# Kernel optimization log

Measured on AMD Instinct MI355X. Metric: run time of the kernel, lower is better.

Reference implementation:

```python
import jax, jax.numpy as jnp
import numpy as np

CONF_THRES = 0.8
NMS_THRES = 0.4
MAX_DET = 300          # fixed capacity for jit-compatible NMS output
N_BOXES = 262144
N_CLASSES = 80


def xywh2xyxy(x):
    xy, wh = x[..., :2], x[..., 2:4]
    return jnp.concatenate([xy - wh * 0.5, xy + wh * 0.5], axis=-1)


def bbox_iou(box, boxes):
    # one box [4] vs many [N,4]; original uses the +1 pixel-area convention
    x1 = jnp.maximum(box[0], boxes[:, 0])
    y1 = jnp.maximum(box[1], boxes[:, 1])
    x2 = jnp.minimum(box[2], boxes[:, 2])
    y2 = jnp.minimum(box[3], boxes[:, 3])
    inter = jnp.clip(x2 - x1 + 1, 0) * jnp.clip(y2 - y1 + 1, 0)
    a1 = (box[2] - box[0] + 1) * (box[3] - box[1] + 1)
    a2 = (boxes[:, 2] - boxes[:, 0] + 1) * (boxes[:, 3] - boxes[:, 1] + 1)
    return inter / (a1 + a2 - inter + 1e-16)


def nms_single(pred):
    # pred: [N, 85] raw YOLO output for one image
    boxes = xywh2xyxy(pred[:, :4])
    obj = pred[:, 4]
    cls_scores = pred[:, 5:]
    class_conf = cls_scores.max(axis=-1)
    class_pred = jnp.argmax(cls_scores, axis=-1).astype(pred.dtype)
    valid = obj >= CONF_THRES
    score = obj * class_conf
    # sort valid boxes by descending score; invalid pushed to the end
    order = jnp.argsort(jnp.where(valid, -score, jnp.inf))
    det = jnp.concatenate(
        [boxes, obj[:, None], class_conf[:, None], class_pred[:, None]], axis=1
    )[order]  # [N, 7] = x1,y1,x2,y2,obj,class_conf,class_pred
    valid = valid[order]

    def step(valid, _):
        idx = jnp.argmax(valid)            # first still-valid (= highest score)
        any_valid = jnp.any(valid)
        cur = det[idx]
        iou = bbox_iou(cur[:4], det[:, :4])
        invalid = (iou > NMS_THRES) & (det[:, 6] == cur[6]) & valid
        # weighted box merge over the suppressed group (as in original NMS)
        w = jnp.where(invalid, det[:, 4], 0.0)
        merged = (w[:, None] * det[:, :4]).sum(0) / (w.sum() + 1e-16)
        out = jnp.where(any_valid,
                        jnp.concatenate([merged, cur[4:]]),
                        jnp.zeros(7, pred.dtype))
        return valid & ~invalid, (out, any_valid)

    _, (kept, kept_valid) = jax.lax.scan(step, valid, None, length=MAX_DET)
    return kept, kept_valid  # [MAX_DET,7], [MAX_DET]


def setup_inputs() -> dict:
    key = jax.random.key(0)
    detections = jax.random.uniform(key, (1, N_BOXES, 5 + N_CLASSES), dtype=jnp.float32)
    return {"detections": detections}


def reference(detections):
    kept, kv = nms_single(detections[0])
    d = kept[:, 5:]                        # [MAX_DET, 2] = (class_conf, class_pred)
    conf_key = jnp.where(kv, d[:, 0], -jnp.inf)  # padded rows sort to the end
    order = jnp.argsort(conf_key)          # ascending (torch argsort)
    d = d[order][::-1]                     # torch.flip -> descending class_conf
    kv = kv[order][::-1]
    probs = jnp.where(kv, d[:, 0], 0.0)    # self.probs
    ids = d[:, 1][None, :]                 # self.ids, shape [1, MAX_DET]
    return ids, probs
```

## Files before the change

kernel.cpp:

```cpp
#include <hip/hip_runtime.h>

#pragma clang fp contract(off)

#define NBOX 262144
#define NCLS 80
#define ROWS 85
#define CAP 1024
#define NSUB 8
#define SUBCAP 128
#define POOL 8192
#define BPT 2
#define S1BOX 512

typedef unsigned long long ull;

__global__ __launch_bounds__(1024) void k_init(int* __restrict__ cnt_pad,
                                               int* __restrict__ pool_count,
                                               int* __restrict__ done_count) {
    const int t = threadIdx.x;
    for (int i = t; i < NCLS * NSUB * 16; i += 1024) cnt_pad[i] = 0;
    if (t == 0) { *pool_count = 0; *done_count = 0; }
}

__global__ __launch_bounds__(256) void k_stage1(const float* __restrict__ det,
                                                int* __restrict__ cnt_pad,
                                                ull* __restrict__ key2,
                                                float* __restrict__ conf2,
                                                float4* __restrict__ box2) {
    __shared__ int s_wl[S1BOX];
    __shared__ float s_obj[S1BOX];
    __shared__ int s_nv;
    const int t = threadIdx.x;
    const int b0 = blockIdx.x * S1BOX;
    const int sb = blockIdx.x & (NSUB - 1);

    if (t == 0) s_nv = 0;
    __syncthreads();

    float obj[BPT];
    #pragma unroll
    for (int i = 0; i < BPT; i++)
        obj[i] = det[(size_t)(b0 + (i << 8) + t) * ROWS + 4];
    #pragma unroll
    for (int i = 0; i < BPT; i++) {
        if (obj[i] >= 0.8f) {
            int r = atomicAdd(&s_nv, 1);
            s_wl[r] = (i << 8) + t;
            s_obj[r] = obj[i];
        }
    }
    __syncthreads();
    const int nv = s_nv;

    const int grp = t >> 4, c = t & 15;
    const int lane = t & 63;
    #pragma unroll 2
    for (int r0 = 0; r0 < nv; r0 += 16) {
        int widx = r0 + grp;
        if (widx < nv) {
            int b = s_wl[widx];
            const float* p = det + (size_t)(b0 + b) * ROWS;
            float aux = (c < 5) ? p[c] : 0.0f;
            float v0 = p[5 + c];
            float v1 = p[21 + c];
            float v2 = p[37 + c];
            float v3 = p[53 + c];
            float v4 = p[69 + c];
            float mv = v0; int mj = c;
            if (v1 > mv) { mv = v1; mj = 16 + c; }
            if (v2 > mv) { mv = v2; mj = 32 + c; }
            if (v3 > mv) { mv = v3; mj = 48 + c; }
            if (v4 > mv) { mv = v4; mj = 64 + c; }
            #pragma unroll
            for (int off = 8; off; off >>= 1) {
                float ov = __shfl_xor(mv, off);
                int oj = __shfl_xor(mj, off);
                if (ov > mv || (ov == mv && oj < mj)) { mv = ov; mj = oj; }
            }
            int gb = lane & 48;
            float x = __shfl(aux, gb + 0);
            float y = __shfl(aux, gb + 1);
            float w = __shfl(aux, gb + 2);
            float h = __shfl(aux, gb + 3);
            if (c == 0) {
                float ob = s_obj[widx];
                float score = ob * mv;
                float hw = w * 0.5f, hh = h * 0.5f;
                int gi = b0 + b;
                int r = atomicAdd(&cnt_pad[((mj * NSUB + sb) << 4)], 1);
                if (r < SUBCAP) {
                    int pos = (mj << 10) + (sb << 7) + r;
                    key2[pos] = ((ull)(~__float_as_uint(score)) << 32) | (unsigned)gi;
                    conf2[pos] = mv;
                    box2[pos] = make_float4(x - hw, y - hh, x + hw, y + hh);
                }
            }
        }
    }
}

template <int L>
__device__ __forceinline__ int exact_alive(ull (&k)[L]) {
    int a = 0;
    #pragma unroll
    for (int j = 0; j < L; j++) a += (int)__popcll(__ballot(k[j] != ~0ULL));
    return a;
}

template <int L>
__device__ __forceinline__ void pick_loop(ull (&k)[L], float4 (&bx)[L], float (&cf)[L],
                                          float (&ar)[L],
                                          int lane, int& alive, int& np,
                                          ull* pkey, float* pconf, int stopAt) {
    while (alive > stopAt && np < 300) {
        ull lm = k[0]; int lj = 0;
        #pragma unroll
        for (int j = 1; j < L; j++) if (k[j] < lm) { lm = k[j]; lj = j; }
        ull gm = lm;
        #pragma unroll
        for (int off = 32; off; off >>= 1) { ull o = __shfl_xor(gm, off); if (o < gm) gm = o; }
        if (gm == ~0ULL) { alive = 0; break; }
        float4 cb = bx[0]; float cc = cf[0];
        #pragma unroll
        for (int j = 1; j < L; j++) if (j == lj) { cb = bx[j]; cc = cf[j]; }
        ull wb = __ballot(lm == gm);
        int wl2 = (int)__ffsll((long long)wb) - 1;
        cb.x = __shfl(cb.x, wl2); cb.y = __shfl(cb.y, wl2);
        cb.z = __shfl(cb.z, wl2); cb.w = __shfl(cb.w, wl2);
        cc = __shfl(cc, wl2);
        if (lane == 0) { pkey[np] = gm; pconf[np] = cc; }
        np++;
        float a1 = (cb.z - cb.x + 1.0f) * (cb.w - cb.y + 1.0f);
        #pragma unroll
        for (int j = 0; j < L; j++) {
            if (k[j] != ~0ULL) {
                float4 b = bx[j];
                float xx1 = fmaxf(cb.x, b.x), yy1 = fmaxf(cb.y, b.y);
                float xx2 = fminf(cb.z, b.z), yy2 = fminf(cb.w, b.w);
                float iw = xx2 - xx1 + 1.0f, ih = yy2 - yy1 + 1.0f;
                float inter = fmaxf(iw, 0.0f) * fmaxf(ih, 0.0f);
                float iou = inter / (a1 + ar[j] - inter + 1e-16f);
                if (iou > 0.4f) k[j] = ~0ULL;
            }
        }
        if ((np & 7) == 0) alive = exact_alive(k);
    }
}

template <int LF, int LT>
__device__ __forceinline__ void compact_regs(ull (&k)[LF], float4 (&bx)[LF], float (&cf)[LF],
                                             ull (&k2)[LT], float4 (&b2)[LT], float (&c2)[LT],
                                             float (&a2)[LT],
                                             int lane, int alive,
                                             ull* dk, float4* db, float* dc) {
    int ci = 0;
    #pragma unroll
    for (int j = 0; j < LF; j++) if (k[j] != ~0ULL) ci++;
    int inc = ci;
    for (int off = 1; off < 64; off <<= 1) {
        int o = __shfl_up(inc, off);
        if (lane >= off) inc += o;
    }
    int wp = inc - ci;
    #pragma unroll
    for (int j = 0; j < LF; j++)
        if (k[j] != ~0ULL) { dk[wp] = k[j]; db[wp] = bx[j]; dc[wp] = cf[j]; wp++; }
    #pragma unroll
    for (int j = 0; j < LT; j++) {
        int pos = lane + (j << 6);
        bool ok = pos < alive;
        k2[j] = ok ? dk[pos] : ~0ULL;
        b2[j] = ok ? db[pos] : make_float4(0.f, 0.f, 0.f, 0.f);
        c2[j] = ok ? dc[pos] : 0.0f;
        a2[j] = (b2[j].z - b2[j].x + 1.0f) * (b2[j].w - b2[j].y + 1.0f);
    }
}

__device__ __forceinline__ void bsort512(ull (&x)[8], int lane) {
    #pragma unroll
    for (int k = 2; k <= 512; k <<= 1) {
        #pragma unroll
        for (int j = k >> 1; j >= 64; j >>= 1) {
            const int jr = j >> 6;
            #pragma unroll
            for (int r2 = 0; r2 < 8; r2++) {
                if ((r2 & jr) == 0) {
                    const bool asc = (((r2 << 6) & k) == 0);
                    ull a = x[r2], b = x[r2 | jr];
                    if ((a > b) == asc) { x[r2] = b; x[r2 | jr] = a; }
                }
            }
        }
        #pragma unroll
        for (int j = ((k >> 1) > 32 ? 32 : (k >> 1)); j >= 1; j >>= 1) {
            #pragma unroll
            for (int r2 = 0; r2 < 8; r2++) {
                int i = (r2 << 6) + lane;
                bool asc = ((i & k) == 0);
                ull o = __shfl_xor(x[r2], j);
                bool lower = ((lane & j) == 0);
                ull mn = x[r2] < o ? x[r2] : o;
                ull mx2 = x[r2] < o ? o : x[r2];
                x[r2] = (asc == lower) ? mn : mx2;
            }
        }
    }
}

__global__ __launch_bounds__(256) void k_nmsfinal(const int* __restrict__ cnt_pad,
                                                  const ull* __restrict__ key2,
                                                  const float* __restrict__ conf2,
                                                  const float4* __restrict__ box2,
                                                  ull* __restrict__ pool_key,
                                                  float* __restrict__ pool_conf,
                                                  int* __restrict__ pool_cls,
                                                  int* __restrict__ pool_count,
                                                  int* __restrict__ done_count,
                                                  float* __restrict__ out) {
    __shared__ ull sk[CAP];
    __shared__ float4 sbx[CAP];
    __shared__ float scf[CAP];
    __shared__ ull pkey[CAP];
    __shared__ float pconf[CAP];
    __shared__ int s_fin;
    __shared__ int s_hist[256];
    __shared__ int s_wt[4];
    __shared__ int s_stat[4];
    __shared__ ull s_buf[512];
    __shared__ unsigned s_cb[512];
    __shared__ unsigned s_cl[512];

    const int c = blockIdx.x, t = threadIdx.x, lane = t & 63, wave = t >> 6;

    if (wave == 0) {
        const int s0 = c << 10;
        int cv0 = 0;
        if (lane < NSUB) cv0 = min(cnt_pad[((c * NSUB + lane) << 4)], SUBCAP);
        int ntot = cv0;
        #pragma unroll
        for (int off = 32; off; off >>= 1) ntot += __shfl_xor(ntot, off);

        ull k16[16]; float4 b16[16]; float c16[16]; float a16[16];
        #pragma unroll
        for (int j = 0; j < 16; j++) {
            int pos = lane + (j << 6);
            int sub = pos >> 7;
            int lim = __shfl(cv0, sub);
            bool ok = (pos & (SUBCAP - 1)) < lim;
            k16[j] = ok ? key2[s0 + pos] : ~0ULL;
            b16[j] = ok ? box2[s0 + pos] : make_float4(0.f, 0.f, 0.f, 0.f);
            c16[j] = ok ? conf2[s0 + pos] : 0.0f;
            a16[j] = (b16[j].z - b16[j].x + 1.0f) * (b16[j].w - b16[j].y + 1.0f);
        }
        int alive = ntot, np = 0;
        pick_loop<16>(k16, b16, c16, a16, lane, alive, np, pkey, pconf, 256);
        alive = exact_alive(k16);
        ull k4[4]; float4 b4[4]; float c4[4]; float a4[4];
        compact_regs<16, 4>(k16, b16, c16, k4, b4, c4, a4, lane, alive, sk, sbx, scf);
        pick_loop<4>(k4, b4, c4, a4, lane, alive, np, pkey, pconf, 64);
        alive = exact_alive(k4);
        ull k1[1]; float4 b1[1]; float c1[1]; float a1r[1];
        compact_regs<4, 1>(k4, b4, c4, k1, b1, c1, a1r, lane, alive, sk, sbx, scf);
        pick_loop<1>(k1, b1, c1, a1r, lane, alive, np, pkey, pconf, 0);

        int npw = min(np, 300);
        int base = 0;
        if (lane == 0 && npw) base = atomicAdd(pool_count, npw);
        base = __shfl(base, 0);
        for (int j = lane; j < npw; j += 64) {
            int pp = base + j;
            if (pp < POOL) {
                ull gm = pkey[j];
                ull pk = ((ull)((unsigned)(gm >> 32) & 0x7FFFFFFFu) << 32)
                       | ((gm & 0xFFFFFFFFull) << 14) | (ull)pp;
                __hip_atomic_store(&pool_key[pp], pk,
                                   __ATOMIC_RELAXED, __HIP_MEMORY_SCOPE_AGENT);
                __hip_atomic_store(&pool_conf[pp], pconf[j],
                                   __ATOMIC_RELAXED, __HIP_MEMORY_SCOPE_AGENT);
                __hip_atomic_store(&pool_cls[pp], c,
                                   __ATOMIC_RELAXED, __HIP_MEMORY_SCOPE_AGENT);
            }
        }
        asm volatile("s_waitcnt vmcnt(0)" ::: "memory");
    }
    __syncthreads();
    if (t == 0) {
        int ticket = atomicAdd(done_count, 1);
        s_fin = (ticket == NCLS - 1) ? 1 : 0;
    }
    __syncthreads();
    if (!s_fin) return;

    const int K = min(__hip_atomic_load(pool_count, __ATOMIC_RELAXED,
                                        __HIP_MEMORY_SCOPE_AGENT), POOL);
    ull key[32];
    #pragma unroll
    for (int j = 0; j < 32; j++) {
        int pos = t + (j << 8);
        key[j] = (pos < K) ? __hip_atomic_load(&pool_key[pos], __ATOMIC_RELAXED,
                                               __HIP_MEMORY_SCOPE_AGENT)
                           : ~0ULL;
    }

    const bool selAll = (K <= 511);
    int sh = 55;
    ull pfin = 0;
    if (!selAll) {
        ull p = 0;
        int gBelow = 0, r = 300;
        while (true) {
            s_hist[t] = 0;
            __syncthreads();
            #pragma unroll
            for (int j = 0; j < 32; j++) {
                ull kk = key[j];
                if ((kk >> (sh + 8)) == p)
                    atomicAdd(&s_hist[(int)((kk >> sh) & 0xFFull)], 1);
            }
            __syncthreads();
            int v = s_hist[t];
            int incv = v;
            for (int off = 1; off < 64; off <<= 1) {
                int o = __shfl_up(incv, off);
                if (lane >= off) incv += o;
            }
            if (lane == 63) s_wt[wave] = incv;
            __syncthreads();
            int wo = 0;
            #pragma unroll
            for (int w2 = 0; w2 < 4; w2++) if (w2 < wave) wo += s_wt[w2];
            int cumIncl = wo + incv;
            int cumExcl = cumIncl - v;
            if (cumExcl < r && r <= cumIncl) {
                s_stat[0] = t; s_stat[1] = cumExcl; s_stat[2] = cumIncl;
            }
            __syncthreads();
            int D = s_stat[0], below = s_stat[1], incl = s_stat[2];
            if (gBelow + incl <= 511 || sh == 7) {
                pfin = (p << 8) | (ull)D;
                break;
            }
            p = (p << 8) | (ull)D;
            gBelow += below;
            r = 300 - gBelow;
            sh -= 8;
            __syncthreads();
        }
    }

    if (t == 0) s_stat[3] = 0;
    __syncthreads();
    int ci = 0;
    #pragma unroll
    for (int j = 0; j < 32; j++) {
        ull kk = key[j];
        bool sel = selAll ? ((kk >> 63) == 0) : ((kk >> sh) <= pfin);
        if (sel) ci++;
    }
    int inc = ci;
    for (int off = 1; off < 64; off <<= 1) {
        int o = __shfl_up(inc, off);
        if (lane >= off) inc += o;
    }
    int wtot = __shfl(inc, 63);
    int wbase2 = 0;
    if (lane == 0 && wtot) wbase2 = atomicAdd(&s_stat[3], wtot);
    wbase2 = __shfl(wbase2, 0);
    int wp = wbase2 + inc - ci;
    #pragma unroll
    for (int j = 0; j < 32; j++) {
        ull kk = key[j];
        bool sel = selAll ? ((kk >> 63) == 0) : ((kk >> sh) <= pfin);
        if (sel) s_buf[wp++] = kk;
    }
    __syncthreads();
    const int S = s_stat[3];
    for (int i = t; i < 512; i += 256) if (i >= S) s_buf[i] = ~0ULL;
    __syncthreads();
    if (wave != 0) return;

    #pragma clang loop unroll(disable)
    for (int pass = 0; pass < 2; pass++) {
        ull x[8];
        #pragma unroll
        for (int r2 = 0; r2 < 8; r2++) x[r2] = s_buf[(r2 << 6) + lane];
        bsort512(x, lane);
        if (pass == 0) {
            #pragma unroll
            for (int r2 = 0; r2 < 8; r2++) {
                int i = (r2 << 6) + lane;
                ull kk = x[r2];
                ull k2 = ~0ULL;
                if (i < 300 && kk != ~0ULL) {
                    int pidx = (int)(kk & 0x3FFFull);
                    unsigned cb = __float_as_uint(
                        __hip_atomic_load(&pool_conf[pidx], __ATOMIC_RELAXED,
                                          __HIP_MEMORY_SCOPE_AGENT));
                    unsigned cl = (unsigned)__hip_atomic_load(&pool_cls[pidx],
                                          __ATOMIC_RELAXED, __HIP_MEMORY_SCOPE_AGENT);
                    s_cb[i] = cb; s_cl[i] = cl;
                    k2 = ((ull)(~cb) << 32) | (unsigned)(~i);
                }
                s_buf[i] = k2;
            }
        } else {
            #pragma unroll
            for (int r2 = 0; r2 < 8; r2++) {
                int i = (r2 << 6) + lane;
                if (i < 300) {
                    ull kk = x[r2];
                    float idv = 0.0f, pv = 0.0f;
                    if (kk != ~0ULL) {
                        int slot = (int)(~(unsigned)(kk & 0xFFFFFFFFull));
                        pv = __uint_as_float(s_cb[slot]);
                        idv = (float)(int)s_cl[slot];
                    }
                    out[i] = idv;
                    out[300 + i] = pv;
                }
            }
        }
    }
}

extern "C" void kernel_launch(void* const* d_in, const int* in_sizes, int n_in,
                              void* d_out, int out_size, void* d_ws, size_t ws_size,
                              hipStream_t stream) {
    const float* det = (const float*)d_in[0];
    float* out = (float*)d_out;
    char* ws = (char*)d_ws;

    int* cnt_pad = (int*)(ws + 0);
    int* pool_count = (int*)(ws + 40960);
    int* done_count = (int*)(ws + 40964);
    ull* key2 = (ull*)(ws + 41024);
    float* conf2 = (float*)(ws + 696384);
    float4* box2 = (float4*)(ws + 1024064);
    ull* pool_key = (ull*)(ws + 2334784);
    float* pool_conf = (float*)(ws + 2400320);
    int* pool_cls = (int*)(ws + 2433088);

    k_init<<<1, 1024, 0, stream>>>(cnt_pad, pool_count, done_count);
    k_stage1<<<NBOX / S1BOX, 256, 0, stream>>>(det, cnt_pad, key2, conf2, box2);
    k_nmsfinal<<<NCLS, 256, 0, stream>>>(cnt_pad, key2, conf2, box2,
                                         pool_key, pool_conf, pool_cls, pool_count,
                                         done_count, out);
}
```

Baseline: 181.7 us.

## Speed up per-class NMS pick loop with tree argmin and 32-bit wave reduce

The per-lane argmin in the NMS pick loop becomes a tree reduction, and the cross-lane min reduces on the high 32 bits of the key first. It falls back to a full 64-bit reduction only when several lanes tie or nothing is left. Input loads are now issued unconditionally before the count read so memory latency overlaps, and the final 4-to-1 compaction stage is dropped in favour of running the 4-wide loop to completion. Shared arrays are also shrunk. The aim is a shorter serial dependency chain per pick, at the cost of more branching and loads of unused slots.

```diff
diff --git a/kernel.cpp b/kernel.cpp
--- a/kernel.cpp
+++ b/kernel.cpp
@@ -113,18 +113,44 @@
                                           int lane, int& alive, int& np,
                                           ull* pkey, float* pconf, int stopAt) {
     while (alive > stopAt && np < 300) {
-        ull lm = k[0]; int lj = 0;
-        #pragma unroll
-        for (int j = 1; j < L; j++) if (k[j] < lm) { lm = k[j]; lj = j; }
-        ull gm = lm;
-        #pragma unroll
-        for (int off = 32; off; off >>= 1) { ull o = __shfl_xor(gm, off); if (o < gm) gm = o; }
-        if (gm == ~0ULL) { alive = 0; break; }
+        ull v[L]; int ix[L];
+        #pragma unroll
+        for (int j = 0; j < L; j++) { v[j] = k[j]; ix[j] = j; }
+        #pragma unroll
+        for (int s = L >> 1; s; s >>= 1) {
+            #pragma unroll
+            for (int j = 0; j < s; j++)
+                if (v[j + s] < v[j]) { v[j] = v[j + s]; ix[j] = ix[j + s]; }
+        }
+        ull lm = v[0]; const int lj = ix[0];
         float4 cb = bx[0]; float cc = cf[0];
         #pragma unroll
         for (int j = 1; j < L; j++) if (j == lj) { cb = bx[j]; cc = cf[j]; }
-        ull wb = __ballot(lm == gm);
-        int wl2 = (int)__ffsll((long long)wb) - 1;
+        unsigned lo = (unsigned)lm;
+        unsigned hi = (unsigned)(lm >> 32);
+        unsigned mh = hi;
+        #pragma unroll
+        for (int off = 32; off; off >>= 1) {
+            unsigned o = __shfl_xor(mh, off);
+            mh = o < mh ? o : mh;
+        }
+        ull wb = __ballot(hi == mh);
+        ull gm; int wl2;
+        if (mh == 0xFFFFFFFFu || __popcll(wb) != 1) {
+            ull g = (hi == mh) ? lm : ~0ULL;
+            #pragma unroll
+            for (int off = 32; off; off >>= 1) {
+                ull o = __shfl_xor(g, off);
+                if (o < g) g = o;
+            }
+            gm = g;
+            if (gm == ~0ULL) { alive = 0; break; }
+            wb = __ballot(lm == gm);
+            wl2 = (int)__ffsll((long long)wb) - 1;
+        } else {
+            wl2 = (int)__ffsll((long long)wb) - 1;
+            gm = ((ull)mh << 32) | (ull)__shfl(lo, wl2);
+        }
         cb.x = __shfl(cb.x, wl2); cb.y = __shfl(cb.y, wl2);
         cb.z = __shfl(cb.z, wl2); cb.w = __shfl(cb.w, wl2);
         cc = __shfl(cc, wl2);
@@ -147,15 +173,14 @@
     }
 }
 
-template <int LF, int LT>
-__device__ __forceinline__ void compact_regs(ull (&k)[LF], float4 (&bx)[LF], float (&cf)[LF],
-                                             ull (&k2)[LT], float4 (&b2)[LT], float (&c2)[LT],
-                                             float (&a2)[LT],
+__device__ __forceinline__ void compact16to4(ull (&k)[16], float4 (&bx)[16], float (&cf)[16],
+                                             ull (&k2)[4], float4 (&b2)[4], float (&c2)[4],
+                                             float (&a2)[4],
                                              int lane, int alive,
                                              ull* dk, float4* db, float* dc) {
     int ci = 0;
     #pragma unroll
-    for (int j = 0; j < LF; j++) if (k[j] != ~0ULL) ci++;
+    for (int j = 0; j < 16; j++) if (k[j] != ~0ULL) ci++;
     int inc = ci;
     for (int off = 1; off < 64; off <<= 1) {
         int o = __shfl_up(inc, off);
@@ -163,10 +188,10 @@
     }
     int wp = inc - ci;
     #pragma unroll
-    for (int j = 0; j < LF; j++)
+    for (int j = 0; j < 16; j++)
         if (k[j] != ~0ULL) { dk[wp] = k[j]; db[wp] = bx[j]; dc[wp] = cf[j]; wp++; }
     #pragma unroll
-    for (int j = 0; j < LT; j++) {
+    for (int j = 0; j < 4; j++) {
         int pos = lane + (j << 6);
         bool ok = pos < alive;
         k2[j] = ok ? dk[pos] : ~0ULL;
@@ -217,11 +242,11 @@
                                                   int* __restrict__ pool_count,
                                                   int* __restrict__ done_count,
                                                   float* __restrict__ out) {
-    __shared__ ull sk[CAP];
-    __shared__ float4 sbx[CAP];
-    __shared__ float scf[CAP];
-    __shared__ ull pkey[CAP];
-    __shared__ float pconf[CAP];
+    __shared__ ull sk[256];
+    __shared__ float4 sbx[256];
+    __shared__ float scf[256];
+    __shared__ ull pkey[304];
+    __shared__ float pconf[304];
     __shared__ int s_fin;
     __shared__ int s_hist[256];
     __shared__ int s_wt[4];
@@ -234,34 +259,41 @@
 
     if (wave == 0) {
         const int s0 = c << 10;
+        ull k16[16]; float4 b16[16]; float c16[16]; float a16[16];
+        #pragma unroll
+        for (int j = 0; j < 16; j++) {
+            int pos = lane + (j << 6);
+            k16[j] = key2[s0 + pos];
+            b16[j] = box2[s0 + pos];
+            c16[j] = conf2[s0 + pos];
+        }
         int cv0 = 0;
         if (lane < NSUB) cv0 = min(cnt_pad[((c * NSUB + lane) << 4)], SUBCAP);
         int ntot = cv0;
         #pragma unroll
         for (int off = 32; off; off >>= 1) ntot += __shfl_xor(ntot, off);
-
-        ull k16[16]; float4 b16[16]; float c16[16]; float a16[16];
         #pragma unroll
         for (int j = 0; j < 16; j++) {
             int pos = lane + (j << 6);
-            int sub = pos >> 7;
-            int lim = __shfl(cv0, sub);
+            int lim = __shfl(cv0, pos >> 7);
             bool ok = (pos & (SUBCAP - 1)) < lim;
-            k16[j] = ok ? key2[s0 + pos] : ~0ULL;
-            b16[j] = ok ? box2[s0 + pos] : make_float4(0.f, 0.f, 0.f, 0.f);
-            c16[j] = ok ? conf2[s0 + pos] : 0.0f;
+            if (!ok) {
+                k16[j] = ~0ULL;
+                b16[j] = make_float4(0.f, 0.f, 0.f, 0.f);
+                c16[j] = 0.0f;
+            }
             a16[j] = (b16[j].z - b16[j].x + 1.0f) * (b16[j].w - b16[j].y + 1.0f);
         }
         int alive = ntot, np = 0;
         pick_loop<16>(k16, b16, c16, a16, lane, alive, np, pkey, pconf, 256);
-        alive = exact_alive(k16);
-        ull k4[4]; float4 b4[4]; float c4[4]; float a4[4];
-        compact_regs<16, 4>(k16, b16, c16, k4, b4, c4, a4, lane, alive, sk, sbx, scf);
-        pick_loop<4>(k4, b4, c4, a4, lane, alive, np, pkey, pconf, 64);
-        alive = exact_alive(k4);
-        ull k1[1]; float4 b1[1]; float c1[1]; float a1r[1];
-        compact_regs<4, 1>(k4, b4, c4, k1, b1, c1, a1r, lane, alive, sk, sbx, scf);
-        pick_loop<1>(k1, b1, c1, a1r, lane, alive, np, pkey, pconf, 0);
+        if (np < 300) {
+            alive = exact_alive(k16);
+            if (alive > 0) {
+                ull k4[4]; float4 b4[4]; float c4[4]; float a4[4];
+                compact16to4(k16, b16, c16, k4, b4, c4, a4, lane, alive, sk, sbx, scf);
+                pick_loop<4>(k4, b4, c4, a4, lane, alive, np, pkey, pconf, 0);
+            }
+        }
 
         int npw = min(np, 300);
         int base = 0;
```

Measured after the change: 179.1 us. No clear change (-1.4%).
